# Kernel optimization log

Measured on AMD Instinct MI355X. Metric: run time of the kernel, lower is better.

Reference implementation:

```python
import jax, jax.numpy as jnp
import numpy as np

H = 1024   # hidden_size
S = 1024   # seq_length
B = 32     # batch_size


def setup_inputs() -> dict:
    key = jax.random.key(0)
    k1, k2, k3, k4, k5, k6 = jax.random.split(key, 6)
    scale = 1.0 / np.sqrt(3 * H)
    return {
        "encoder_states": jax.random.normal(k1, (S, B, 2 * H), dtype=jnp.float32),
        "hidden": jax.random.normal(k2, (B, H), dtype=jnp.float32),
        "cell": jax.random.normal(k3, (B, H), dtype=jnp.float32),
        "W_attn": jax.random.normal(k4, (H, 3 * H), dtype=jnp.float32) * scale,
        "b_attn": jax.random.normal(k5, (H,), dtype=jnp.float32) * scale,
        "v_w": jax.random.normal(k6, (H,), dtype=jnp.float32) * (1.0 / np.sqrt(H)),
    }


def reference(encoder_states, hidden, cell, W_attn, b_attn, v_w):
    # cell is accepted by the original forward but unused.
    # Split the concat-linear into two projections (mathematically identical,
    # avoids materializing the repeated hidden + concat tensor):
    # cat((hidden_rep, enc), -1) @ W.T == hidden @ W[:, :H].T + enc @ W[:, H:].T
    W_h = W_attn[:, :H]          # [H, H]   multiplies decoder hidden
    W_e = W_attn[:, H:]          # [H, 2H]  multiplies encoder states
    enc = jnp.transpose(encoder_states, (1, 0, 2))          # [B, S, 2H]
    h_proj = hidden @ W_h.T + b_attn                         # [B, H], broadcast over S
    e_proj = jnp.einsum("bse,he->bsh", enc, W_e)             # [B, S, H]
    energy = jnp.tanh(h_proj[:, None, :] + e_proj)           # [B, S, H]
    attention = jnp.einsum("bsh,h->bs", energy, v_w)         # [B, S]
    return jax.nn.softmax(attention, axis=1)
```

## Files before the change

kernel.cpp:

```cpp
#include <hip/hip_runtime.h>
#include <hip/hip_bf16.h>

#define H 1024
#define S 1024
#define B 32
#define K2 2048

typedef unsigned short u16;
typedef __attribute__((ext_vector_type(8))) short short8;
typedef __attribute__((ext_vector_type(8))) unsigned short u16x8;
typedef __attribute__((ext_vector_type(4))) float floatx4;

__device__ __forceinline__ u16 f2bf(float f) {
  unsigned u = __float_as_uint(f);
  u += 0x7FFFu + ((u >> 16) & 1u);
  return (u16)(u >> 16);
}

__device__ __forceinline__ void gld_lds16(const void* g, void* l) {
  __builtin_amdgcn_global_load_lds(
      (const __attribute__((address_space(1))) unsigned int*)g,
      (__attribute__((address_space(3))) unsigned int*)l, 16, 0, 0);
}

__device__ __forceinline__ unsigned cvt_pk(float lo, float hi) {
  __hip_bfloat162 h = __float22bfloat162_rn(float2{lo, hi});
  return *(unsigned*)&h;
}

__device__ __forceinline__ short8 mk_frag(floatx4 lo, floatx4 hi) {
  union { unsigned u[4]; short8 s; } r;
  r.u[0] = cvt_pk(lo[0], lo[1]);
  r.u[1] = cvt_pk(lo[2], lo[3]);
  r.u[2] = cvt_pk(hi[0], hi[1]);
  r.u[3] = cvt_pk(hi[2], hi[3]);
  return r.s;
}

__global__ void conv_we_k(const float* __restrict__ W, u16* __restrict__ dst) {
  const int h = blockIdx.x;
  const int t = threadIdx.x * 8;
  const float* sp = W + (size_t)h * 3072 + H + t;
  u16* dp = dst + (size_t)h * K2 + t;
  floatx4 x = *(const floatx4*)sp;
  floatx4 y = *(const floatx4*)(sp + 4);
  u16x8 o;
  o[0] = f2bf(x[0]); o[1] = f2bf(x[1]); o[2] = f2bf(x[2]); o[3] = f2bf(x[3]);
  o[4] = f2bf(y[0]); o[5] = f2bf(y[1]); o[6] = f2bf(y[2]); o[7] = f2bf(y[3]);
  *(u16x8*)dp = o;
}

__global__ void hproj_k(const float* __restrict__ hidden, const float* __restrict__ W,
                        const float* __restrict__ b_attn, float* __restrict__ hp) {
  const int lane = threadIdx.x & 63;
  const int h = (blockIdx.x * blockDim.x + threadIdx.x) >> 6;
  float wr[16];
#pragma unroll
  for (int i = 0; i < 16; i++) wr[i] = W[(size_t)h * 3072 + lane + i * 64];
  for (int b = 0; b < B; b++) {
    float d = 0.f;
#pragma unroll
    for (int i = 0; i < 16; i++) d = fmaf(wr[i], hidden[b * H + lane + i * 64], d);
#pragma unroll
    for (int off = 32; off; off >>= 1) d += __shfl_xor(d, off);
    if (lane == 0) hp[b * H + h] = d + b_attn[h];
  }
}

#define BM 128
#define BN 128
#define BK 32

__global__ __launch_bounds__(256) void gemm_fused_k(
    const float* __restrict__ enc,
    const u16* __restrict__ Bw,
    const float* __restrict__ hp, const float* __restrict__ vw,
    float* __restrict__ attn) {
  __shared__ __align__(16) float sA[BM * 32];
  __shared__ __align__(16) u16 sB[BN * BK];
  const int tid = threadIdx.x;
  const int bid = blockIdx.x;
  const int ntile = bid >> 8;
  const int b = (bid & 255) >> 3;
  const int mtile = bid & 7;
  const int s0 = mtile * BM;
  const int h0 = ntile * BN;

  const int lane = tid & 63;
  const int wv = tid >> 6;
  const int wm = (wv >> 1) * 64;
  const int wn = (wv & 1) * 64;
  const int fr = lane & 15;
  const int kgrp = lane >> 4;

  const int lr8 = lane >> 3, sg8 = lane & 7;
  const int lr4 = lane >> 2, sg4 = lane & 3;

  floatx4 acc[4][4];
#pragma unroll
  for (int i = 0; i < 4; i++)
#pragma unroll
    for (int j = 0; j < 4; j++) acc[i][j] = (floatx4){0.f, 0.f, 0.f, 0.f};

  for (int k0 = 0; k0 < K2; k0 += BK) {
    __syncthreads();
#pragma unroll
    for (int p = 0; p < 4; p++) {
      const int r = wv * 32 + p * 8 + lr8;
      gld_lds16(enc + ((size_t)(s0 + r) * B + b) * K2 + k0 + ((sg8 ^ (r & 7)) << 2),
                (char*)sA + (wv * 32 + p * 8) * 128);
    }
#pragma unroll
    for (int p = 0; p < 2; p++) {
      const int r = wv * 32 + p * 16 + lr4;
      gld_lds16(Bw + (size_t)(h0 + r) * K2 + k0 + ((sg4 ^ ((r >> 1) & 3)) << 3),
                (char*)sB + (wv * 32 + p * 16) * 64);
    }
    __syncthreads();

    short8 af[4], bf[4];
#pragma unroll
    for (int mf = 0; mf < 4; mf++) {
      const int R = wm + mf * 16 + fr;
      const int f7 = R & 7;
      floatx4 lo = *(const floatx4*)&sA[R * 32 + ((((kgrp << 1)) ^ f7) << 2)];
      floatx4 hi = *(const floatx4*)&sA[R * 32 + ((((kgrp << 1) | 1) ^ f7) << 2)];
      af[mf] = mk_frag(lo, hi);
    }
#pragma unroll
    for (int nf = 0; nf < 4; nf++) {
      const int R = wn + nf * 16 + fr;
      bf[nf] = *(const short8*)&sB[R * BK + ((kgrp ^ ((R >> 1) & 3)) << 3)];
    }
#pragma unroll
    for (int mf = 0; mf < 4; mf++)
#pragma unroll
      for (int nf = 0; nf < 4; nf++)
        acc[mf][nf] =
            __builtin_amdgcn_mfma_f32_16x16x32_bf16(af[mf], bf[nf], acc[mf][nf], 0, 0, 0);
  }

  const int col = fr;
  const int rgrp = lane >> 4;
  float hv[4], vv[4];
#pragma unroll
  for (int nf = 0; nf < 4; nf++) {
    const int h = h0 + wn + nf * 16 + col;
    hv[nf] = hp[b * H + h];
    vv[nf] = vw[h];
  }
#pragma unroll
  for (int mf = 0; mf < 4; mf++) {
#pragma unroll
    for (int r = 0; r < 4; r++) {
      float part = 0.f;
#pragma unroll
      for (int nf = 0; nf < 4; nf++) part += tanhf(acc[mf][nf][r] + hv[nf]) * vv[nf];
      part += __shfl_xor(part, 1);
      part += __shfl_xor(part, 2);
      part += __shfl_xor(part, 4);
      part += __shfl_xor(part, 8);
      if (col == 0)
        atomicAdd(&attn[b * S + s0 + wm + mf * 16 + rgrp * 4 + r], part);
    }
  }
}

__global__ void softmax_k(const float* __restrict__ attn, float* __restrict__ out) {
  __shared__ float red[8];
  const int b = blockIdx.x;
  const int tid = threadIdx.x;
  const float* row = attn + b * S;
  float v[4];
#pragma unroll
  for (int i = 0; i < 4; i++) v[i] = row[tid + i * 256];
  float m = fmaxf(fmaxf(v[0], v[1]), fmaxf(v[2], v[3]));
#pragma unroll
  for (int off = 32; off; off >>= 1) m = fmaxf(m, __shfl_xor(m, off));
  if ((tid & 63) == 0) red[tid >> 6] = m;
  __syncthreads();
  m = fmaxf(fmaxf(red[0], red[1]), fmaxf(red[2], red[3]));
  float e[4], sum = 0.f;
#pragma unroll
  for (int i = 0; i < 4; i++) { e[i] = __expf(v[i] - m); sum += e[i]; }
#pragma unroll
  for (int off = 32; off; off >>= 1) sum += __shfl_xor(sum, off);
  __syncthreads();
  if ((tid & 63) == 0) red[4 + (tid >> 6)] = sum;
  __syncthreads();
  sum = red[4] + red[5] + red[6] + red[7];
  const float inv = 1.0f / sum;
#pragma unroll
  for (int i = 0; i < 4; i++) out[b * S + tid + i * 256] = e[i] * inv;
}

extern "C" void kernel_launch(void* const* d_in, const int* in_sizes, int n_in,
                              void* d_out, int out_size, void* d_ws, size_t ws_size,
                              hipStream_t stream) {
  const float* enc    = (const float*)d_in[0];
  const float* hidden = (const float*)d_in[1];
  const float* W_attn = (const float*)d_in[3];
  const float* b_attn = (const float*)d_in[4];
  const float* v_w    = (const float*)d_in[5];
  float* out = (float*)d_out;

  char* ws = (char*)d_ws;
  float* attn = (float*)ws;
  float* hp   = (float*)(ws + 131072);
  u16* Web    = (u16*)(ws + 262144);

  hipMemsetAsync(attn, 0, B * S * sizeof(float), stream);
  conv_we_k<<<H, 256, 0, stream>>>(W_attn, Web);
  hproj_k<<<256, 256, 0, stream>>>(hidden, W_attn, b_attn, hp);
  gemm_fused_k<<<2048, 256, 0, stream>>>(enc, Web, hp, v_w, attn);
  softmax_k<<<B, 256, 0, stream>>>(attn, out);
}
```

Measured before the change: 607.8 us.

## Register-prefetch A tile, convert to bf16 before LDS, double BK, fast tanh

Result: slower. 777.9 us (+28.0%).

```diff
diff --git a/kernel.cpp b/kernel.cpp
--- a/kernel.cpp
+++ b/kernel.cpp
@@ -28,13 +28,11 @@
   return *(unsigned*)&h;
 }
 
-__device__ __forceinline__ short8 mk_frag(floatx4 lo, floatx4 hi) {
-  union { unsigned u[4]; short8 s; } r;
-  r.u[0] = cvt_pk(lo[0], lo[1]);
-  r.u[1] = cvt_pk(lo[2], lo[3]);
-  r.u[2] = cvt_pk(hi[0], hi[1]);
-  r.u[3] = cvt_pk(hi[2], hi[3]);
-  return r.s;
+__device__ __forceinline__ float fast_tanh(float x) {
+  float ax = __builtin_fabsf(x);
+  float t = __expf(-2.f * ax);
+  float r = (1.f - t) * __builtin_amdgcn_rcpf(1.f + t);
+  return __builtin_copysignf(r, x);
 }
 
 __global__ void conv_we_k(const float* __restrict__ W, u16* __restrict__ dst) {
@@ -69,14 +67,15 @@
 
 #define BM 128
 #define BN 128
-#define BK 32
+#define BK 64
+#define LDA 72
 
 __global__ __launch_bounds__(256) void gemm_fused_k(
     const float* __restrict__ enc,
     const u16* __restrict__ Bw,
     const float* __restrict__ hp, const float* __restrict__ vw,
     float* __restrict__ attn) {
-  __shared__ __align__(16) float sA[BM * 32];
+  __shared__ __align__(16) u16 sA[BM * LDA];
   __shared__ __align__(16) u16 sB[BN * BK];
   const int tid = threadIdx.x;
   const int bid = blockIdx.x;
@@ -93,51 +92,69 @@
   const int fr = lane & 15;
   const int kgrp = lane >> 4;
 
-  const int lr8 = lane >> 3, sg8 = lane & 7;
-  const int lr4 = lane >> 2, sg4 = lane & 3;
+  const int ar = tid >> 1;
+  const int ah = tid & 1;
+  const float* aG = enc + ((size_t)(s0 + ar) * B + b) * K2 + ah * 32;
+  const int lr8 = lane >> 3;
+  const int sg8 = lane & 7;
 
   floatx4 acc[4][4];
 #pragma unroll
   for (int i = 0; i < 4; i++)
 #pragma unroll
     for (int j = 0; j < 4; j++) acc[i][j] = (floatx4){0.f, 0.f, 0.f, 0.f};
+
+  floatx4 av[8];
+#pragma unroll
+  for (int j = 0; j < 8; j++) av[j] = *(const floatx4*)(aG + j * 4);
 
   for (int k0 = 0; k0 < K2; k0 += BK) {
     __syncthreads();
 #pragma unroll
     for (int p = 0; p < 4; p++) {
       const int r = wv * 32 + p * 8 + lr8;
-      gld_lds16(enc + ((size_t)(s0 + r) * B + b) * K2 + k0 + ((sg8 ^ (r & 7)) << 2),
-                (char*)sA + (wv * 32 + p * 8) * 128);
-    }
-#pragma unroll
-    for (int p = 0; p < 2; p++) {
-      const int r = wv * 32 + p * 16 + lr4;
-      gld_lds16(Bw + (size_t)(h0 + r) * K2 + k0 + ((sg4 ^ ((r >> 1) & 3)) << 3),
-                (char*)sB + (wv * 32 + p * 16) * 64);
+      gld_lds16(Bw + (size_t)(h0 + r) * K2 + k0 + ((sg8 ^ (r & 7)) << 3),
+                (char*)sB + (wv * 32 + p * 8) * 128);
+    }
+    {
+      union { unsigned u[16]; u16x8 v[4]; } aw;
+#pragma unroll
+      for (int j = 0; j < 8; j++) {
+        aw.u[2 * j]     = cvt_pk(av[j][0], av[j][1]);
+        aw.u[2 * j + 1] = cvt_pk(av[j][2], av[j][3]);
+      }
+      u16* adst = &sA[ar * LDA + ah * 32];
+#pragma unroll
+      for (int j = 0; j < 4; j++) *(u16x8*)(adst + j * 8) = aw.v[j];
     }
     __syncthreads();
 
-    short8 af[4], bf[4];
-#pragma unroll
-    for (int mf = 0; mf < 4; mf++) {
-      const int R = wm + mf * 16 + fr;
-      const int f7 = R & 7;
-      floatx4 lo = *(const floatx4*)&sA[R * 32 + ((((kgrp << 1)) ^ f7) << 2)];
-      floatx4 hi = *(const floatx4*)&sA[R * 32 + ((((kgrp << 1) | 1) ^ f7) << 2)];
-      af[mf] = mk_frag(lo, hi);
-    }
-#pragma unroll
-    for (int nf = 0; nf < 4; nf++) {
-      const int R = wn + nf * 16 + fr;
-      bf[nf] = *(const short8*)&sB[R * BK + ((kgrp ^ ((R >> 1) & 3)) << 3)];
-    }
-#pragma unroll
-    for (int mf = 0; mf < 4; mf++)
-#pragma unroll
-      for (int nf = 0; nf < 4; nf++)
-        acc[mf][nf] =
-            __builtin_amdgcn_mfma_f32_16x16x32_bf16(af[mf], bf[nf], acc[mf][nf], 0, 0, 0);
+    {
+      const int kn = (k0 + BK < K2) ? (k0 + BK) : 0;
+#pragma unroll
+      for (int j = 0; j < 8; j++) av[j] = *(const floatx4*)(aG + kn + j * 4);
+    }
+
+#pragma unroll
+    for (int j = 0; j < 2; j++) {
+      short8 af[4], bfv[4];
+#pragma unroll
+      for (int mf = 0; mf < 4; mf++) {
+        const int R = wm + mf * 16 + fr;
+        af[mf] = *(const short8*)&sA[R * LDA + j * 32 + kgrp * 8];
+      }
+#pragma unroll
+      for (int nf = 0; nf < 4; nf++) {
+        const int R = wn + nf * 16 + fr;
+        bfv[nf] = *(const short8*)&sB[R * BK + ((((j << 2) + kgrp) ^ (R & 7)) << 3)];
+      }
+#pragma unroll
+      for (int mf = 0; mf < 4; mf++)
+#pragma unroll
+        for (int nf = 0; nf < 4; nf++)
+          acc[mf][nf] =
+              __builtin_amdgcn_mfma_f32_16x16x32_bf16(af[mf], bfv[nf], acc[mf][nf], 0, 0, 0);
+    }
   }
 
   const int col = fr;
@@ -155,7 +172,7 @@
     for (int r = 0; r < 4; r++) {
       float part = 0.f;
 #pragma unroll
-      for (int nf = 0; nf < 4; nf++) part += tanhf(acc[mf][nf][r] + hv[nf]) * vv[nf];
+      for (int nf = 0; nf < 4; nf++) part += fast_tanh(acc[mf][nf][r] + hv[nf]) * vv[nf];
       part += __shfl_xor(part, 1);
       part += __shfl_xor(part, 2);
       part += __shfl_xor(part, 4);
```
